# Performance work log

Hardware: AMD Instinct MI355X
Metric: run time of the kernel (lower is better)

The kernel has to match this reference:

```python
import jax, jax.numpy as jnp
import numpy as np

D = 768; HID = 3072; FFN = 2048; NH = 8; NL = 2; T = 64; V = 50257; B = 16
ALPHA = 0.4; HD = D // NH

def _gelu(x):
    return jax.nn.gelu(x, approximate=False)

def _ln(x, g, b, eps=1e-5):
    m = x.mean(-1, keepdims=True)
    v = x.var(-1, keepdims=True)
    return (x - m) / jnp.sqrt(v + eps) * g + b

def _l2norm(x):
    return x / jnp.maximum(jnp.linalg.norm(x, axis=-1, keepdims=True), 1e-12)

def _mha(x, in_w, in_b, out_w, out_b, mask):
    b, t, _ = x.shape
    qkv = x @ in_w.T + in_b
    q, k, v = jnp.split(qkv, 3, axis=-1)
    q = q.reshape(b, t, NH, HD); k = k.reshape(b, t, NH, HD); v = v.reshape(b, t, NH, HD)
    s = jnp.einsum('bqhd,bkhd->bhqk', q, k) / jnp.sqrt(jnp.asarray(HD, jnp.float32))
    s = jnp.where(mask[None, None], -jnp.inf, s)
    a = jax.nn.softmax(s, axis=-1)
    o = jnp.einsum('bhqk,bkhd->bqhd', a, v).reshape(b, t, D)
    return o @ out_w.T + out_b

def _forward(token_ids, emb, pos_emb, attn_in_w, attn_in_b, attn_out_w, attn_out_b,
             ff_w1, ff_b1, ff_w2, ff_b2, n1_g, n1_b, n2_g, n2_b, enc_norm_g, enc_norm_b,
             V0, b0, V1, b1, cp_w1, cp_b1, cp_w2, cp_b2, gate_w, gate_b, temp_w, R,
             out_g, out_b, lm_head):
    sg = jax.lax.stop_gradient
    x = emb[token_ids] + pos_emb[None, :token_ids.shape[1]]
    t = token_ids.shape[1]
    mask = jnp.triu(jnp.ones((t, t), bool), 1)
    for l in range(NL):
        xn = _ln(x, n1_g[l], n1_b[l])
        x = x + _mha(xn, attn_in_w[l], attn_in_b[l], attn_out_w[l], attn_out_b[l], mask)
        xn = _ln(x, n2_g[l], n2_b[l])
        x = x + _gelu(xn @ ff_w1[l].T + ff_b1[l]) @ ff_w2[l].T + ff_b2[l]
    ctx = _l2norm(_ln(x, enc_norm_g, enc_norm_b))  # [B,T,D]

    def step(h_prev, ctx_t):
        h_d = sg(h_prev)                      # h_prev.detach()
        traw = h_d @ R                        # temporal_raw
        tc = ctx_t + ALPHA * traw             # temporal_context
        # differentiable shadow path through hierarchy weights V0,b0,V1,b1
        h_sh = _gelu(tc @ V0 + b0)
        core_sh = _l2norm(_gelu(h_sh @ V1 + b1))
        # settled state: hierarchy inference under no_grad (settle approximated
        # by the same feedforward pass; fully stop-gradiented like x.detach())
        tcd = sg(tc)
        core_set = sg(_l2norm(_gelu(_gelu(tcd @ V0 + b0) @ V1 + b1)))
        blend = 0.5 * core_sh + 0.5 * core_set
        cf = _gelu(blend @ cp_w1.T + cp_b1) @ cp_w2.T + cp_b2   # core_proj
        tf = traw @ temp_w.T                                     # temporal_proj
        gate = jax.nn.sigmoid(jnp.concatenate([ctx_t, cf], -1) @ gate_w.T + gate_b)
        h_t = gate * (cf + ALPHA * tf) + (1.0 - gate) * ctx_t    # gate_warmup=1.0
        h_t = jnp.clip(_ln(h_t, out_g, out_b), -5.0, 5.0)
        return sg(h_t), h_t @ lm_head.T

    h0 = jnp.zeros((token_ids.shape[0], D), jnp.float32)
    _, logits = jax.lax.scan(step, h0, jnp.swapaxes(ctx, 0, 1))
    return jnp.transpose(logits, (1, 0, 2))

def setup_inputs():
    key = jax.random.key(0)
    ks = iter(jax.random.split(key, 64))
    def nrm(shape, s=0.02):
        return jax.random.normal(next(ks), shape, jnp.float32) * s
    return {
        'token_ids': jax.random.randint(next(ks), (B, T), 0, V),
        'emb': nrm((V, D)),
        'pos_emb': nrm((T, D)),
        'attn_in_w': nrm((NL, 3 * D, D)),
        'attn_in_b': jnp.zeros((NL, 3 * D), jnp.float32),
        'attn_out_w': nrm((NL, D, D)),
        'attn_out_b': jnp.zeros((NL, D), jnp.float32),
        'ff_w1': nrm((NL, FFN, D)),
        'ff_b1': jnp.zeros((NL, FFN), jnp.float32),
        'ff_w2': nrm((NL, D, FFN)),
        'ff_b2': jnp.zeros((NL, D), jnp.float32),
        'n1_g': jnp.ones((NL, D), jnp.float32),
        'n1_b': jnp.zeros((NL, D), jnp.float32),
        'n2_g': jnp.ones((NL, D), jnp.float32),
        'n2_b': jnp.zeros((NL, D), jnp.float32),
        'enc_norm_g': jnp.ones((D,), jnp.float32),
        'enc_norm_b': jnp.zeros((D,), jnp.float32),
        'V0': nrm((D, HID)),
        'b0': jnp.zeros((HID,), jnp.float32),
        'V1': nrm((HID, D)),
        'b1': jnp.zeros((D,), jnp.float32),
        'cp_w1': nrm((D, D)),
        'cp_b1': jnp.zeros((D,), jnp.float32),
        'cp_w2': nrm((D, D)),
        'cp_b2': jnp.zeros((D,), jnp.float32),
        'gate_w': nrm((D, 2 * D)),
        'gate_b': jnp.zeros((D,), jnp.float32),
        'temp_w': nrm((D, D)),
        'R': nrm((D, D), 0.1),
        'out_g': jnp.ones((D,), jnp.float32),
        'out_b': jnp.zeros((D,), jnp.float32),
        'lm_head': nrm((V, D)),
    }

def reference(token_ids, emb, pos_emb, attn_in_w, attn_in_b, attn_out_w, attn_out_b,
              ff_w1, ff_b1, ff_w2, ff_b2, n1_g, n1_b, n2_g, n2_b, enc_norm_g, enc_norm_b,
              V0, b0, V1, b1, cp_w1, cp_b1, cp_w2, cp_b2, gate_w, gate_b, temp_w, R,
              out_g, out_b, lm_head):
    return _forward(token_ids, emb, pos_emb, attn_in_w, attn_in_b, attn_out_w, attn_out_b,
                    ff_w1, ff_b1, ff_w2, ff_b2, n1_g, n1_b, n2_g, n2_b, enc_norm_g, enc_norm_b,
                    V0, b0, V1, b1, cp_w1, cp_b1, cp_w2, cp_b2, gate_w, gate_b, temp_w, R,
                    out_g, out_b, lm_head)
```

## Files before the change

### kernel.cpp

```cpp
#include <hip/hip_runtime.h>
#include <math.h>

typedef _Float16 f16;
typedef f16 f16x8 __attribute__((ext_vector_type(8)));
typedef f16 f16x4 __attribute__((ext_vector_type(4)));
typedef float f32x4 __attribute__((ext_vector_type(4)));
typedef unsigned int u32;
typedef unsigned long long u64;

#define TT 64
#define DD 768
#define MR 1024
#define ALPHAF 0.4f
#define NWG 120
#define GRID 240
#define LMN 50257
#define LMK 768

__device__ __forceinline__ float geluf(float x){
  return 0.5f*x*(1.0f + erff(x*0.70710678118654752f));
}

__device__ __forceinline__ u64 ld_a64(const void* p){
  return __hip_atomic_load((const u64*)p, __ATOMIC_RELAXED, __HIP_MEMORY_SCOPE_AGENT);
}
__device__ __forceinline__ f16x8 ld_act16h(const f16* p){
  union { u64 u[2]; f16x8 v; } c;
  c.u[0] = ld_a64(p); c.u[1] = ld_a64(p + 4); return c.v;
}
__device__ __forceinline__ float ld_actf(const float* p){
  union { u32 u; float f; } c;
  c.u = __hip_atomic_load((const u32*)p, __ATOMIC_RELAXED, __HIP_MEMORY_SCOPE_AGENT);
  return c.f;
}
__device__ __forceinline__ void st_actf(float* p, float v){
  union { u32 u; float f; } c; c.f = v;
  __hip_atomic_store((u32*)p, c.u, __ATOMIC_RELAXED, __HIP_MEMORY_SCOPE_AGENT);
}
__device__ __forceinline__ void st_acth(f16* p, float v){
  union { unsigned short u; f16 h; } c; c.h = (f16)v;
  __hip_atomic_store((unsigned short*)p, c.u, __ATOMIC_RELAXED, __HIP_MEMORY_SCOPE_AGENT);
}

__device__ __forceinline__ void egbar(int* ef, int ep){
  __syncthreads();
  if (threadIdx.x == 0){
    __threadfence();
    __hip_atomic_store(ef + blockIdx.x*32, ep, __ATOMIC_RELAXED, __HIP_MEMORY_SCOPE_AGENT);
  }
  {
    int id = threadIdx.x; bool active = id < GRID;
    const int* fp = ef + id*32;
    while (true){
      int v = active ? __hip_atomic_load(fp, __ATOMIC_RELAXED, __HIP_MEMORY_SCOPE_AGENT) : ep;
      if (__ballot(v >= ep) == ~0ull) break;
      __builtin_amdgcn_s_sleep(1);
    }
  }
  __syncthreads();
  if (threadIdx.x == 0) __threadfence();
  __syncthreads();
}

__device__ __forceinline__ void postf(int* f, int ep){
  asm volatile("s_waitcnt vmcnt(0)" ::: "memory");
  __syncthreads();
  if (threadIdx.x == 0)
    __hip_atomic_store(f, ep, __ATOMIC_RELAXED, __HIP_MEMORY_SCOPE_AGENT);
}
__device__ __forceinline__ void waitf(const int* f, int n, int ep){
  if (threadIdx.x < 64){
    int lane = threadIdx.x;
    while (true){
      bool ok = true;
      for (int i = lane; i < n; i += 64){
        if (__hip_atomic_load(f + i*32, __ATOMIC_RELAXED, __HIP_MEMORY_SCOPE_AGENT) < ep){
          ok = false; break;
        }
      }
      if (__ballot(ok) == ~0ull) break;
      __builtin_amdgcn_s_sleep(1);
    }
  }
  __syncthreads();
}

__device__ __forceinline__ void red_store(float* rb, int lane, f32x4 a){
  rb[lane] = a[0]; rb[64+lane] = a[1]; rb[128+lane] = a[2]; rb[192+lane] = a[3];
}
__device__ __forceinline__ f32x4 red_sum4(float rb[4][256], int lane){
  f32x4 s;
  #pragma unroll
  for (int r = 0; r < 4; r++)
    s[r] = rb[0][r*64+lane] + rb[1][r*64+lane] + rb[2][r*64+lane] + rb[3][r*64+lane];
  return s;
}
__device__ __forceinline__ f32x4 red_sum2(float rb[4][256], int lane, int w0, int w1){
  f32x4 s;
  #pragma unroll
  for (int r = 0; r < 4; r++)
    s[r] = rb[w0][r*64+lane] + rb[w1][r*64+lane];
  return s;
}

__device__ void dev_ln(const float* xr, const float* g, const float* b,
                       float* outr, float* outTr, float* red, bool l2n){
  int tid = threadIdx.x, lane = tid & 63, wid = tid >> 6;
  float v[3]; float s = 0.f, ss = 0.f;
  #pragma unroll
  for (int j = 0; j < 3; j++){ float t0 = xr[tid + j*256]; v[j] = t0; s += t0; ss += t0*t0; }
  #pragma unroll
  for (int o = 1; o < 64; o <<= 1){ s += __shfl_xor(s, o); ss += __shfl_xor(ss, o); }
  if (lane == 0){ red[wid] = s; red[4+wid] = ss; }
  __syncthreads();
  s  = red[0]+red[1]+red[2]+red[3];
  ss = red[4]+red[5]+red[6]+red[7];
  float mean = s*(1.f/768.f);
  float var  = ss*(1.f/768.f) - mean*mean;
  float rstd = rsqrtf(var + 1e-5f);
  float y[3];
  #pragma unroll
  for (int j = 0; j < 3; j++){ int n = tid + j*256; y[j] = (v[j]-mean)*rstd*g[n] + b[n]; }
  if (l2n){
    float n2 = y[0]*y[0] + y[1]*y[1] + y[2]*y[2];
    #pragma unroll
    for (int o = 1; o < 64; o <<= 1) n2 += __shfl_xor(n2, o);
    __syncthreads();
    if (lane == 0) red[wid] = n2;
    __syncthreads();
    n2 = red[0]+red[1]+red[2]+red[3];
    float inv = 1.f / fmaxf(sqrtf(n2), 1e-12f);
    y[0] *= inv; y[1] *= inv; y[2] *= inv;
  }
  #pragma unroll
  for (int j = 0; j < 3; j++) outr[tid + j*256] = y[j];
  if (outTr){
    #pragma unroll
    for (int j = 0; j < 3; j++) outTr[tid + j*256] = y[j];
  }
  __syncthreads();
}

__device__ void dev_gemm_tile(char* lds, const float* A, int lda,
    const float* Bw, int ldb, int nrb, int N, int K, int m0, int n0,
    const float* bias, const float* res, float* outF, f16* outH,
    float scale, int act, int operm)
{
  int tid = threadIdx.x;
  int lane = tid & 63, wid = tid >> 6;
  int wr = (wid >> 1)*64, wc = (wid & 1)*64;
  int l15 = lane & 15, kb = lane >> 4;
  f32x4 acc[4][4];
  #pragma unroll
  for (int i = 0; i < 4; i++)
    #pragma unroll
    for (int j = 0; j < 4; j++){ f32x4 z = {0.f,0.f,0.f,0.f}; acc[i][j] = z; }
  int rA = tid >> 3;
  int k4 = (tid & 7)*4;
  float4 va[4], vb[4];
  #pragma unroll
  for (int it = 0; it < 4; ++it){
    int r = it*32 + rA;
    va[it] = *(const float4*)(A + (size_t)(m0+r)*lda + k4);
    int rB = n0 + r;
    if (rB < nrb) vb[it] = *(const float4*)(Bw + (size_t)rB*ldb + k4);
    else { vb[it].x=0.f; vb[it].y=0.f; vb[it].z=0.f; vb[it].w=0.f; }
  }
  for (int kk = 0; kk < K; kk += 32){
    char* cb = lds + (((kk >> 5) & 1) ? 20480 : 0);
    f16 (*As)[40] = (f16(*)[40])cb;
    f16 (*Bs)[40] = (f16(*)[40])(cb + 10240);
    #pragma unroll
    for (int it = 0; it < 4; ++it){
      int r = it*32 + rA;
      *(f16x4*)(&As[r][k4]) = (f16x4){(f16)va[it].x,(f16)va[it].y,(f16)va[it].z,(f16)va[it].w};
      *(f16x4*)(&Bs[r][k4]) = (f16x4){(f16)vb[it].x,(f16)vb[it].y,(f16)vb[it].z,(f16)vb[it].w};
    }
    __syncthreads();
    if (kk + 32 < K){
      #pragma unroll
      for (int it = 0; it < 4; ++it){
        int r = it*32 + rA;
        va[it] = *(const float4*)(A + (size_t)(m0+r)*lda + kk + 32 + k4);
        int rB = n0 + r;
        if (rB < nrb) vb[it] = *(const float4*)(Bw + (size_t)rB*ldb + kk + 32 + k4);
        else { vb[it].x=0.f; vb[it].y=0.f; vb[it].z=0.f; vb[it].w=0.f; }
      }
    }
    f16x8 af[4], bfv[4];
    #pragma unroll
    for (int i = 0; i < 4; i++) af[i]  = *(const f16x8*)(&As[wr + i*16 + l15][kb*8]);
    #pragma unroll
    for (int j = 0; j < 4; j++) bfv[j] = *(const f16x8*)(&Bs[wc + j*16 + l15][kb*8]);
    #pragma unroll
    for (int i = 0; i < 4; i++)
      #pragma unroll
      for (int j = 0; j < 4; j++)
        acc[i][j] = __builtin_amdgcn_mfma_f32_16x16x32_f16(af[i], bfv[j], acc[i][j], 0, 0, 0);
  }
  __syncthreads();
  #pragma unroll
  for (int i = 0; i < 4; i++){
    #pragma unroll
    for (int j = 0; j < 4; j++){
      #pragma unroll
      for (int r = 0; r < 4; r++){
        int m = m0 + wr + i*16 + kb*4 + r;
        int n = n0 + wc + j*16 + l15;
        if (n < N){
          float v = acc[i][j][r]*scale;
          if (bias) v += bias[n];
          if (act == 1) v = geluf(v);
          if (res) v += res[(size_t)m*N + n];
          size_t off;
          if (operm == 0) off = (size_t)m*N + n;
          else            off = ((size_t)(m & 63)*16 + (m >> 6))*N + n;
          if (outF) outF[off] = v;
          if (outH) outH[off] = (f16)v;
        }
      }
    }
  }
}

__device__ void dev_attn(char* lds, const float* qkv, float* o, int bh){
  float (*kv)[96] = (float(*)[96])lds;
  float (*sm)[68] = (float(*)[68])(lds + 24576);
  int b = bh >> 3, h = bh & 7;
  int tid = threadIdx.x;
  const float* base = qkv + (size_t)b*64*2304 + h*96;
  for (int idx = tid; idx < 64*96; idx += 256){ int i = idx/96, d = idx - i*96;
    kv[i][d] = base[(size_t)i*2304 + 768 + d]; }
  __syncthreads();
  {
    int i = tid >> 2;
    const float* q = base + (size_t)i*2304;
    int j0 = (tid & 3)*16;
    for (int jj = 0; jj < 16; jj++){
      int j = j0 + jj;
      float sv = -1e30f;
      if (j <= i){ float acc = 0.f;
        for (int d = 0; d < 96; d++) acc += q[d]*kv[j][d];
        sv = acc*0.10206207261596576f; }
      sm[i][j] = sv;
    }
  }
  __syncthreads();
  for (int idx = tid; idx < 64*96; idx += 256){ int i = idx/96, d = idx - i*96;
    kv[i][d] = base[(size_t)i*2304 + 1536 + d]; }
  if (tid < 64){
    int i = tid;
    float mx = -1e30f;
    for (int j = 0; j <= i; j++) mx = fmaxf(mx, sm[i][j]);
    float sum = 0.f;
    for (int j = 0; j <= i; j++){ float e = expf(sm[i][j]-mx); sm[i][j] = e; sum += e; }
    float inv = 1.f/sum;
    for (int j = 0; j <= i; j++) sm[i][j] *= inv;
  }
  __syncthreads();
  for (int idx = tid; idx < 64*96; idx += 256){
    int i = idx/96, d = idx - i*96;
    float acc = 0.f;
    for (int j = 0; j <= i; j++) acc += sm[i][j]*kv[j][d];
    o[(size_t)(b*64+i)*768 + h*96 + d] = acc;
  }
  __syncthreads();
}

__device__ void dev_tr_f(char* lds, const float* in, float* out, int R, int C, int bx, int by){
  float (*tile)[33] = (float(*)[33])lds;
  int r0 = by*32, c0 = bx*32;
  int tx = threadIdx.x & 31, ty = threadIdx.x >> 5;
  #pragma unroll
  for (int i = 0; i < 32; i += 8) tile[ty+i][tx] = in[(size_t)(r0+ty+i)*C + (c0+tx)];
  __syncthreads();
  #pragma unroll
  for (int i = 0; i < 32; i += 8) out[(size_t)(c0+ty+i)*R + (r0+tx)] = tile[tx][ty+i];
  __syncthreads();
}
__device__ void dev_tr_h(char* lds, const float* in, f16* out, int R, int C, int bx, int by){
  float (*tile)[33] = (float(*)[33])lds;
  int r0 = by*32, c0 = bx*32;
  int tx = threadIdx.x & 31, ty = threadIdx.x >> 5;
  #pragma unroll
  for (int i = 0; i < 32; i += 8) tile[ty+i][tx] = in[(size_t)(r0+ty+i)*C + (c0+tx)];
  __syncthreads();
  #pragma unroll
  for (int i = 0; i < 32; i += 8) out[(size_t)(c0+ty+i)*R + (r0+tx)] = (f16)tile[tx][ty+i];
  __syncthreads();
}

__global__ void k_init(int* flags){
  for (int i = threadIdx.x; i < 512*32; i += 256) flags[i] = 0;
}

__global__ __launch_bounds__(256, 1) void k_all(
  const int* tok, const float* emb, const float* pos,
  const float* aiw, const float* aib, const float* aow, const float* aob,
  const float* fw1, const float* fb1, const float* fw2, const float* fb2,
  const float* n1g, const float* n1b, const float* n2g, const float* n2b,
  const float* eng, const float* enb,
  const float* V0, const float* b0, const float* V1, const float* b1,
  const float* cw1, const float* cb1, const float* cw2, const float* cb2,
  const float* gw, const float* gb_, const float* tw, const float* Rm,
  const float* og, const float* ob, const float* lmw,
  float* x, float* xn, float* qkv, float* o_, float* mid,
  float* ctx, float* ctxT, float* V0t, float* cw2t,
  float* ctxV0T, float* gctxT, float* bdg,
  f16* WAf, f16* V1tf, f16* Wc1f, f16* WDf, f16* lmw16,
  f16* hf, f16* h1f, f16* c1f, f16* gcaf,
  float* cf, float* gpre, float* tfs, int* flags, float* out)
{
  __shared__ __align__(16) char smem[147456];
  __shared__ float redbuf[4][256];
  __shared__ float normp[4][16];
  __shared__ float red[8];
  const int tid = threadIdx.x, lane = tid & 63, wid = tid >> 6;
  const int bid = blockIdx.x;
  const int l15 = lane & 15, kb = lane >> 4;
  int* afl = flags;
  int* bfl = flags + 120*32;
  int* cfl = flags + 168*32;
  int* dfl = flags + 192*32;
  int* mfl = flags + 240*32;
  int* encf = flags + 256*32;
  int eep = 0;

  for (int m = bid; m < MR; m += GRID){
    int t = m & 63; int id = tok[m];
    const float* e = emb + (size_t)id*DD;
    const float* p = pos + (size_t)t*DD;
    float* xr = x + (size_t)m*DD;
    for (int j = tid; j < DD; j += 256) xr[j] = e[j] + p[j];
  }
  egbar(encf, ++eep);

  for (int l = 0; l < 2; l++){
    for (int m = bid; m < MR; m += GRID)
      dev_ln(x + (size_t)m*DD, n1g + l*DD, n1b + l*DD, xn + (size_t)m*DD, nullptr, red, false);
    egbar(encf, ++eep);
    for (int tl = bid; tl < 144; tl += GRID)
      dev_gemm_tile(smem, xn, 768, aiw + (size_t)l*2304*768, 768, 2304, 2304, 768,
                    (tl % 8)*128, (tl / 8)*128, aib + l*2304, nullptr, qkv, nullptr, 1.f, 0, 0);
    egbar(encf, ++eep);
    for (int u = bid; u < 128; u += GRID) dev_attn(smem, qkv, o_, u);
    egbar(encf, ++eep);
    for (int tl = bid; tl < 48; tl += GRID)
      dev_gemm_tile(smem, o_, 768, aow + (size_t)l*768*768, 768, 768, 768, 768,
                    (tl % 8)*128, (tl / 8)*128, aob + l*768, x, x, nullptr, 1.f, 0, 0);
    egbar(encf, ++eep);
    for (int m = bid; m < MR; m += GRID)
      dev_ln(x + (size_t)m*DD, n2g + l*DD, n2b + l*DD, xn + (size_t)m*DD, nullptr, red, false);
    egbar(encf, ++eep);
    for (int tl = bid; tl < 128; tl += GRID)
      dev_gemm_tile(smem, xn, 768, fw1 + (size_t)l*2048*768, 768, 2048, 2048, 768,
                    (tl % 8)*128, (tl / 8)*128, fb1 + l*2048, nullptr, mid, nullptr, 1.f, 1, 0);
    egbar(encf, ++eep);
    for (int tl = bid; tl < 48; tl += GRID)
      dev_gemm_tile(smem, mid, 2048, fw2 + (size_t)l*768*2048, 2048, 768, 768, 2048,
                    (tl % 8)*128, (tl / 8)*128, fb2 + l*768, x, x, nullptr, 1.f, 0, 0);
    egbar(encf, ++eep);
  }
  for (int m = bid; m < MR; m += GRID)
    dev_ln(x + (size_t)m*DD, eng, enb, ctx + (size_t)m*DD,
           ctxT + ((size_t)(m & 63)*16 + (m >> 6))*DD, red, true);
  egbar(encf, ++eep);

  for (int task = bid; task < 5184; task += GRID){
    if (task < 2304)      dev_tr_f(smem, V0, V0t, 768, 3072, task % 96, task / 96);
    else if (task < 2880){ int t2 = task - 2304; dev_tr_f(smem, cw2, cw2t, 768, 768, t2 % 24, t2 / 24); }
    else                 { int t2 = task - 2880; dev_tr_h(smem, V1, V1tf, 3072, 768, t2 % 24, t2 / 24); }
  }
  {
    const int g0 = bid*256 + tid, stride = GRID*256;
    for (int i = g0; i < 73728; i += stride){
      float4 a = ((const float4*)cw1)[i*2]; float4 b2 = ((const float4*)cw1)[i*2+1];
      ((f16x8*)Wc1f)[i] = (f16x8){(f16)a.x,(f16)a.y,(f16)a.z,(f16)a.w,(f16)b2.x,(f16)b2.y,(f16)b2.z,(f16)b2.w};
    }
    for (int i = g0; i < 73728; i += stride){
      float4 a = ((const float4*)cw2)[i*2]; float4 b2 = ((const float4*)cw2)[i*2+1];
      ((f16x8*)WDf)[i] = (f16x8){(f16)a.x,(f16)a.y,(f16)a.z,(f16)a.w,(f16)b2.x,(f16)b2.y,(f16)b2.z,(f16)b2.w};
    }
    for (int g = g0; g < 768; g += stride){
      const float* row = gw + (size_t)g*1536 + 768;
      float s = 0.f;
      for (int j = 0; j < 768; j++) s += cb2[j]*row[j];
      bdg[g] = s;
    }
  }
  egbar(encf, ++eep);

  for (int task = bid; task < 456; task += GRID){
    if (task < 144)
      dev_gemm_tile(smem, V0t, 768, Rm, 768, 768, 768, 768,
                    (task % 24)*128, (task / 24)*128, nullptr, nullptr, nullptr, WAf, ALPHAF, 0, 0);
    else if (task < 180){ int t2 = task - 144;
      dev_gemm_tile(smem, tw, 768, Rm, 768, 768, 768, 768,
                    (t2 % 6)*128, (t2 / 6)*128, nullptr, nullptr, nullptr, WAf + (size_t)3072*768, ALPHAF, 0, 0); }
    else if (task < 372){ int t2 = task - 180;
      dev_gemm_tile(smem, ctx, 768, V0t, 768, 3072, 3072, 768,
                    (t2 % 8)*128, (t2 / 8)*128, b0, nullptr, ctxV0T, nullptr, 1.f, 0, 1); }
    else if (task < 420){ int t2 = task - 372;
      dev_gemm_tile(smem, ctx, 768, gw, 1536, 768, 768, 768,
                    (t2 % 8)*128, (t2 / 8)*128, nullptr, nullptr, gctxT, nullptr, 1.f, 0, 1); }
    else { int t2 = task - 420;
      dev_gemm_tile(smem, gw + 768, 1536, cw2t, 768, 768, 768, 768,
                    (t2 % 6)*128, (t2 / 6)*128, nullptr, nullptr, nullptr, WDf + (size_t)768*768, 1.f, 0, 0); }
  }
  egbar(encf, ++eep);

  if (bid >= NWG){
    const int lw = bid - NWG;
    const int wr = (wid >> 1)*64, wc = (wid & 1)*64;
    for (int nt = lw; nt < 393; nt += 120){
      int r0 = nt*128;
      int rend = r0 + 128; if (rend > LMN) rend = LMN;
      int u0 = r0*96, u1 = rend*96;
      for (int i = u0 + tid; i < u1; i += 256){
        float4 a = ((const float4*)lmw)[(size_t)i*2];
        float4 b2 = ((const float4*)lmw)[(size_t)i*2+1];
        ((f16x8*)lmw16)[i] = (f16x8){(f16)a.x,(f16)a.y,(f16)a.z,(f16)a.w,
                                     (f16)b2.x,(f16)b2.y,(f16)b2.z,(f16)b2.w};
      }
    }
    __syncthreads();
    for (int q = 0; q < 8; ++q){
      waitf(mfl, 16, q*8 + 8);
      size_t arow[4];
      #pragma unroll
      for (int i = 0; i < 4; i++){
        int rl = wr + i*16 + l15;
        arow[i] = ((size_t)(rl >> 3)*TT + q*8 + (rl & 7))*DD + kb*8;
      }
      for (int nt = lw; nt < 393; nt += 120){
        int n0 = nt*128;
        size_t brow[4];
        #pragma unroll
        for (int j = 0; j < 4; j++){
          int n = n0 + wc + j*16 + l15;
          if (n > LMN-1) n = LMN-1;
          brow[j] = (size_t)n*LMK + kb*8;
        }
        f32x4 acc[4][4];
        #pragma unroll
        for (int i = 0; i < 4; i++)
          #pragma unroll
          for (int j = 0; j < 4; j++){ f32x4 z = {0.f,0.f,0.f,0.f}; acc[i][j] = z; }
        #pragma unroll 4
        for (int kk = 0; kk < LMK; kk += 32){
          f16x8 af[4], bf[4];
          #pragma unroll
          for (int i = 0; i < 4; i++) af[i] = ld_act16h(hf + arow[i] + kk);
          #pragma unroll
          for (int j = 0; j < 4; j++) bf[j] = *(const f16x8*)(lmw16 + brow[j] + kk);
          #pragma unroll
          for (int i = 0; i < 4; i++)
            #pragma unroll
            for (int j = 0; j < 4; j++)
              acc[i][j] = __builtin_amdgcn_mfma_f32_16x16x32_f16(af[i], bf[j], acc[i][j], 0, 0, 0);
        }
        #pragma unroll
        for (int i = 0; i < 4; i++){
          #pragma unroll
          for (int j = 0; j < 4; j++){
            #pragma unroll
            for (int r = 0; r < 4; r++){
              int ml = wr + i*16 + kb*4 + r;
              int b = ml >> 3, tt = q*8 + (ml & 7);
              int n = n0 + wc + j*16 + l15;
              if (n < LMN) out[((size_t)b*TT + tt)*LMN + n] = acc[i][j][r];
            }
          }
        }
      }
    }
    return;
  }

  {
    const f16* src = WAf + (size_t)bid*32*768;
    for (int c = tid; c < 3072; c += 256){
      int row = c/96, kc = c - row*96;
      int off = (row*1536 + kc*16) ^ ((row&7)<<4);
      *(f16x8*)(smem + off) = *(const f16x8*)(src + (size_t)row*768 + kc*8);
    }
    if (bid < 48){
      const f16* s2 = V1tf + (size_t)bid*16*3072;
      for (int c = tid; c < 6144; c += 256){
        int row = c/384, kc = c - row*384;
        int off = (row*6144 + kc*16) ^ ((row&7)<<4);
        *(f16x8*)(smem + 49152 + off) = *(const f16x8*)(s2 + (size_t)row*3072 + kc*8);
      }
    } else if (bid < 72){
      const f16* s2 = Wc1f + (size_t)(bid-48)*32*768;
      for (int c = tid; c < 3072; c += 256){
        int row = c/96, kc = c - row*96;
        int off = (row*1536 + kc*16) ^ ((row&7)<<4);
        *(f16x8*)(smem + 49152 + off) = *(const f16x8*)(s2 + (size_t)row*768 + kc*8);
      }
    } else {
      const f16* s2 = WDf + (size_t)(bid-72)*32*768;
      for (int c = tid; c < 3072; c += 256){
        int row = c/96, kc = c - row*96;
        int off = (row*1536 + kc*16) ^ ((row&7)<<4);
        *(f16x8*)(smem + 49152 + off) = *(const f16x8*)(s2 + (size_t)row*768 + kc*8);
      }
    }
  }
  __syncthreads();

  const int n_a = bid*32 + (wid>>1)*16 + l15;
  float b1v = 0.f;
  if (bid < 48) b1v = b1[bid*16 + l15];
  float cpb1v = 0.f;
  if (bid >= 48 && bid < 72) cpb1v = cb1[((bid-48)*2 + (wid>>1))*16 + l15];
  float dbv = 0.f; int n_d = 0;
  if (bid >= 72){
    n_d = ((bid-72)*2 + (wid>>1))*16 + l15;
    dbv = (n_d < 768) ? cb2[n_d] : bdg[n_d - 768];
  }
  float gb3[3], og3[3], ob3[3];
  if (bid < 16){
    #pragma unroll
    for (int j = 0; j < 3; j++){
      int n = tid + j*256;
      gb3[j] = gb_[n]; og3[j] = og[n]; ob3[j] = ob[n];
    }
  }

  for (int t = 0; t < TT; ++t){
    const int ep = t + 1;
    f32x4 cv = {0.f,0.f,0.f,0.f};
    if ((wid & 1) == 0 && n_a < 3072){
      const float* p = ctxV0T + (size_t)t*16*3072 + n_a;
      #pragma unroll
      for (int r = 0; r < 4; r++) cv[r] = p[(size_t)(kb*4+r)*3072];
    }

    if (t > 0) waitf(mfl, 16, t);
    {
      const int u = wid >> 1, kh = wid & 1;
      const int k0 = kh*384 + kb*8;
      f32x4 a = {0.f,0.f,0.f,0.f};
      if (t > 0){
        const f16* ap = hf + ((size_t)l15*TT + (t-1))*DD + k0;
        const int row = u*16 + l15, rowoff = row*1536, sw = (row&7)<<4;
        #pragma unroll
        for (int b = 0; b < 12; b++){
          int wb = (rowoff + (k0 + b*32)*2) ^ sw;
          f16x8 vb = *(const f16x8*)(smem + wb);
          f16x8 va = ld_act16h(ap + b*32);
          a = __builtin_amdgcn_mfma_f32_16x16x32_f16(va, vb, a, 0,0,0);
        }
      }
      red_store(redbuf[wid], lane, a);
    }
    __syncthreads();
    if ((wid & 1) == 0){
      f32x4 s4 = red_sum2(redbuf, lane, wid, wid+1);
      #pragma unroll
      for (int r = 0; r < 4; r++){
        int m = kb*4 + r;
        if (n_a < 3072){
          float hv = geluf(s4[r] + cv[r]);
          st_acth(h1f + (size_t)m*3072 + n_a, hv);
        } else {
          st_actf(tfs + m*DD + (n_a - 3072), s4[r]);
        }
      }
    }
    postf(afl + bid*32, ep);
    if (bid < 48){
      waitf(afl, 120, ep);
      const int k0 = wid*768 + kb*8;
      const f16* ap = h1f + (size_t)l15*3072 + k0;
      const int rowoff = l15*6144, sw = (l15&7)<<4;
      f32x4 a = {0.f,0.f,0.f,0.f};
      #pragma unroll
      for (int b = 0; b < 24; b++){
        int wb = (rowoff + (k0 + b*32)*2) ^ sw;
        f16x8 vb = *(const f16x8*)(smem + 49152 + wb);
        f16x8 va = ld_act16h(ap + b*32);
        a = __builtin_amdgcn_mfma_f32_16x16x32_f16(va, vb, a, 0,0,0);
      }
      red_store(redbuf[wid], lane, a);
      __syncthreads();
      if (wid == 0){
        f32x4 s4 = red_sum4(redbuf, lane);
        int n = bid*16 + l15;
        #pragma unroll
        for (int r = 0; r < 4; r++){
          int m = kb*4 + r;
          st_acth(c1f + (size_t)m*DD + n, geluf(s4[r] + b1v));
        }
      }
      postf(bfl + bid*32, ep);
    }
    float gv[3], cxv[3];
    if (bid < 16){
      #pragma unroll
      for (int j = 0; j < 3; j++){
        size_t o2 = ((size_t)t*16 + bid)*DD + tid + j*256;
        gv[j] = gctxT[o2]; cxv[j] = ctxT[o2];
      }
    }
    if (bid >= 48 && bid < 72){
      waitf(bfl, 48, ep);
      const int u = wid >> 1, kh = wid & 1;
      const int k0 = kh*384 + kb*8;
      const f16* ap = c1f + (size_t)l15*DD + k0;
      const int row = u*16 + l15, rowoff = row*1536, sw = (row&7)<<4;
      f32x4 a = {0.f,0.f,0.f,0.f};
      float sq = 0.f;
      #pragma unroll
      for (int b = 0; b < 12; b++){
        int wb = (rowoff + (k0 + b*32)*2) ^ sw;
        f16x8 vb = *(const f16x8*)(smem + 49152 + wb);
        f16x8 va = ld_act16h(ap + b*32);
        a = __builtin_amdgcn_mfma_f32_16x16x32_f16(va, vb, a, 0,0,0);
        #pragma unroll
        for (int j = 0; j < 8; j++){ float xv = (float)va[j]; sq = fmaf(xv, xv, sq); }
      }
      sq += __shfl_xor(sq,16); sq += __shfl_xor(sq,32);
      if (lane < 16) normp[wid][lane] = sq;
      red_store(redbuf[wid], lane, a);
      __syncthreads();
      if ((wid & 1) == 0){
        f32x4 s4 = red_sum2(redbuf, lane, wid, wid+1);
        int n = ((bid-48)*2 + (wid>>1))*16 + l15;
        #pragma unroll
        for (int r = 0; r < 4; r++){
          int m = kb*4 + r;
          float nm = normp[wid][m] + normp[wid+1][m];
          float inv = 1.f / fmaxf(sqrtf(nm), 1e-12f);
          st_acth(gcaf + (size_t)m*DD + n, geluf(s4[r]*inv + cpb1v));
        }
      }
      postf(cfl + (bid-48)*32, ep);
    }
    if (bid >= 72){
      waitf(cfl, 24, ep);
      const int u = wid >> 1, kh = wid & 1;
      const int k0 = kh*384 + kb*8;
      const f16* ap = gcaf + (size_t)l15*DD + k0;
      const int row = u*16 + l15, rowoff = row*1536, sw = (row&7)<<4;
      f32x4 a = {0.f,0.f,0.f,0.f};
      #pragma unroll
      for (int b = 0; b < 12; b++){
        int wb = (rowoff + (k0 + b*32)*2) ^ sw;
        f16x8 vb = *(const f16x8*)(smem + 49152 + wb);
        f16x8 va = ld_act16h(ap + b*32);
        a = __builtin_amdgcn_mfma_f32_16x16x32_f16(va, vb, a, 0,0,0);
      }
      red_store(redbuf[wid], lane, a);
      __syncthreads();
      if ((wid & 1) == 0){
        f32x4 s4 = red_sum2(redbuf, lane, wid, wid+1);
        #pragma unroll
        for (int r = 0; r < 4; r++){
          int m = kb*4 + r;
          if (n_d < 768) st_actf(cf + m*DD + n_d, s4[r] + dbv);
          else           st_actf(gpre + m*DD + (n_d - 768), s4[r] + dbv);
        }
      }
      postf(dfl + (bid-72)*32, ep);
    }
    if (bid < 16){
      waitf(dfl, 48, ep);
      int m = bid;
      float vals[3]; float s = 0.f, ss = 0.f;
      #pragma unroll
      for (int j = 0; j < 3; j++){
        int n = tid + j*256;
        float gi = gv[j] + ld_actf(gpre + m*DD + n) + gb3[j];
        float gate = 1.f/(1.f + expf(-gi));
        float v = gate*(ld_actf(cf + m*DD + n) + ld_actf(tfs + m*DD + n)) + (1.f - gate)*cxv[j];
        vals[j] = v; s += v; ss += v*v;
      }
      #pragma unroll
      for (int o2 = 1; o2 < 64; o2 <<= 1){ s += __shfl_xor(s, o2); ss += __shfl_xor(ss, o2); }
      if (lane == 0){ red[wid] = s; red[4+wid] = ss; }
      __syncthreads();
      s  = red[0]+red[1]+red[2]+red[3];
      ss = red[4]+red[5]+red[6]+red[7];
      float mean = s*(1.f/768.f), var = ss*(1.f/768.f) - mean*mean;
      float rstd = rsqrtf(var + 1e-5f);
      #pragma unroll
      for (int j = 0; j < 3; j++){
        int n = tid + j*256;
        float y = (vals[j]-mean)*rstd*og3[j] + ob3[j];
        y = fminf(5.f, fmaxf(-5.f, y));
        st_acth(hf + ((size_t)m*TT + t)*DD + n, y);
      }
      postf(mfl + bid*32, ep);
    }
  }
}

extern "C" void kernel_launch(void* const* d_in, const int* in_sizes, int n_in,
                              void* d_out, int out_size, void* d_ws, size_t ws_size,
                              hipStream_t stream)
{
  (void)in_sizes; (void)n_in; (void)out_size; (void)ws_size;
  const int*   tok = (const int*)d_in[0];
  const float* emb = (const float*)d_in[1];
  const float* pos = (const float*)d_in[2];
  const float* aiw = (const float*)d_in[3];
  const float* aib = (const float*)d_in[4];
  const float* aow = (const float*)d_in[5];
  const float* aob = (const float*)d_in[6];
  const float* fw1 = (const float*)d_in[7];
  const float* fb1 = (const float*)d_in[8];
  const float* fw2 = (const float*)d_in[9];
  const float* fb2 = (const float*)d_in[10];
  const float* n1g = (const float*)d_in[11];
  const float* n1b = (const float*)d_in[12];
  const float* n2g = (const float*)d_in[13];
  const float* n2b = (const float*)d_in[14];
  const float* eng = (const float*)d_in[15];
  const float* enb = (const float*)d_in[16];
  const float* V0  = (const float*)d_in[17];
  const float* b0  = (const float*)d_in[18];
  const float* V1  = (const float*)d_in[19];
  const float* b1  = (const float*)d_in[20];
  const float* cw1 = (const float*)d_in[21];
  const float* cb1 = (const float*)d_in[22];
  const float* cw2 = (const float*)d_in[23];
  const float* cb2 = (const float*)d_in[24];
  const float* gw  = (const float*)d_in[25];
  const float* gb  = (const float*)d_in[26];
  const float* tw  = (const float*)d_in[27];
  const float* Rm  = (const float*)d_in[28];
  const float* og  = (const float*)d_in[29];
  const float* ob  = (const float*)d_in[30];
  const float* lmw = (const float*)d_in[31];
  float* out = (float*)d_out;

  char* base = (char*)d_ws; size_t off = 0;
  auto alloc = [&](size_t bytes)->void*{
    off = (off + 255) & ~(size_t)255; void* p = base + off; off += bytes; return p; };

  float* x     = (float*)alloc((size_t)MR*DD*4);
  float* xn    = (float*)alloc((size_t)MR*DD*4);
  float* qkv   = (float*)alloc((size_t)MR*2304*4);
  float* o_    = (float*)alloc((size_t)MR*DD*4);
  float* mid   = (float*)alloc((size_t)MR*2048*4);
  float* ctx   = (float*)alloc((size_t)MR*DD*4);
  float* ctxT  = (float*)alloc((size_t)MR*DD*4);
  float* V0t   = (float*)alloc((size_t)3072*768*4);
  float* cw2t  = (float*)alloc((size_t)768*768*4);
  float* ctxV0T= (float*)alloc((size_t)MR*3072*4);
  float* gctxT = (float*)alloc((size_t)MR*DD*4);
  float* bdg   = (float*)alloc(768*4);
  f16*   WAf   = (f16*)alloc((size_t)3840*768*2);
  f16*   V1tf  = (f16*)alloc((size_t)768*3072*2);
  f16*   Wc1f  = (f16*)alloc((size_t)768*768*2);
  f16*   WDf   = (f16*)alloc((size_t)1536*768*2);
  f16*   lmw16 = (f16*)alloc((size_t)LMN*768*2);
  f16*   hf    = (f16*)alloc((size_t)MR*DD*2);
  f16*   h1f   = (f16*)alloc((size_t)16*3072*2);
  f16*   c1f   = (f16*)alloc((size_t)16*768*2);
  f16*   gcaf  = (f16*)alloc((size_t)16*768*2);
  float* cf    = (float*)alloc((size_t)16*768*4);
  float* gpre  = (float*)alloc((size_t)16*768*4);
  float* tfs   = (float*)alloc((size_t)16*768*4);
  int*   flags = (int*)alloc((size_t)512*32*4);

  k_init<<<1, 256, 0, stream>>>(flags);
  k_all<<<GRID, 256, 0, stream>>>(tok, emb, pos, aiw, aib, aow, aob,
      fw1, fb1, fw2, fb2, n1g, n1b, n2g, n2b, eng, enb,
      V0, b0, V1, b1, cw1, cb1, cw2, cb2, gw, gb, tw, Rm, og, ob, lmw,
      x, xn, qkv, o_, mid, ctx, ctxT, V0t, cw2t, ctxV0T, gctxT, bdg,
      WAf, V1tf, Wc1f, WDf, lmw16, hf, h1f, c1f, gcaf, cf, gpre, tfs, flags, out);
}
```

Before: 2.698 ms.

## Fuse gating and LayerNorm partial stats into D-stage, remove serial epilogue barrier

The gate, blend and partial LayerNorm sums are now computed inside the D-stage workgroups. Each writes its values and per-slice sum/sumsq into a 4-slot ring buffer. The next timestep's A-stage reconstructs mean/rstd from those partials and applies the LayerNorm on the fly while loading its MFMA operand. This removes one cross-workgroup barrier hop per recurrent step, the separate 16-block LN stage. The LM-head workgroups now materialise hf for the lm_head GEMM off the critical path. The cost is extra redundant LN arithmetic in the A-stage, a ring-buffer dependency (D waits on mfl t-3), and a less stable variance formula.

```diff
diff --git a/kernel.cpp b/kernel.cpp
--- a/kernel.cpp
+++ b/kernel.cpp
@@ -27,6 +27,9 @@
 __device__ __forceinline__ f16x8 ld_act16h(const f16* p){
   union { u64 u[2]; f16x8 v; } c;
   c.u[0] = ld_a64(p); c.u[1] = ld_a64(p + 4); return c.v;
+}
+__device__ __forceinline__ float2 ld_actf2(const float* p){
+  union { u64 u; float2 f; } c; c.u = ld_a64(p); return c.f;
 }
 __device__ __forceinline__ float ld_actf(const float* p){
   union { u32 u; float f; } c;
@@ -309,7 +312,7 @@
   float* ctxV0T, float* gctxT, float* bdg,
   f16* WAf, f16* V1tf, f16* Wc1f, f16* WDf, f16* lmw16,
   f16* hf, f16* h1f, f16* c1f, f16* gcaf,
-  float* cf, float* gpre, float* tfs, int* flags, float* out)
+  float* val, float* pp, float* tfs, int* flags, float* out)
 {
   __shared__ __align__(16) char smem[147456];
   __shared__ float redbuf[4][256];
@@ -424,53 +427,131 @@
       }
     }
     __syncthreads();
-    for (int q = 0; q < 8; ++q){
-      waitf(mfl, 16, q*8 + 8);
-      size_t arow[4];
-      #pragma unroll
-      for (int i = 0; i < 4; i++){
-        int rl = wr + i*16 + l15;
-        arow[i] = ((size_t)(rl >> 3)*TT + q*8 + (rl & 7))*DD + kb*8;
-      }
-      for (int nt = lw; nt < 393; nt += 120){
-        int n0 = nt*128;
-        size_t brow[4];
+
+    if (lw < 16){
+      const int m = lw;
+      for (int t = 0; t < TT; ++t){
+        waitf(dfl, 48, t+1);
+        const int slot = t & 3;
+        if (tid < 64){
+          float s = 0.f, ss = 0.f;
+          if (lane < 48){
+            float2 v2 = ld_actf2(pp + slot*1536 + m*96 + lane*2);
+            s = v2.x; ss = v2.y;
+          }
+          #pragma unroll
+          for (int o2 = 1; o2 < 64; o2 <<= 1){ s += __shfl_xor(s, o2); ss += __shfl_xor(ss, o2); }
+          if (lane == 0){ red[0] = s; red[1] = ss; }
+        }
+        __syncthreads();
+        float mean = red[0]*(1.f/768.f);
+        float rstd = rsqrtf(red[1]*(1.f/768.f) - mean*mean + 1e-5f);
         #pragma unroll
-        for (int j = 0; j < 4; j++){
-          int n = n0 + wc + j*16 + l15;
-          if (n > LMN-1) n = LMN-1;
-          brow[j] = (size_t)n*LMK + kb*8;
-        }
-        f32x4 acc[4][4];
+        for (int j = 0; j < 3; j++){
+          int n = tid + j*256;
+          float v = ld_actf(val + slot*12288 + m*768 + n);
+          float y = (v - mean)*rstd*og[n] + ob[n];
+          y = fminf(5.f, fmaxf(-5.f, y));
+          st_acth(hf + ((size_t)m*TT + t)*DD + n, y);
+        }
+        postf(mfl + m*32, t+1);
+        if ((t & 7) == 7){
+          int q = t >> 3;
+          waitf(mfl, 16, t+1);
+          size_t arow[4];
+          #pragma unroll
+          for (int i = 0; i < 4; i++){
+            int rl = wr + i*16 + l15;
+            arow[i] = ((size_t)(rl >> 3)*TT + q*8 + (rl & 7))*DD + kb*8;
+          }
+          for (int nt = lw; nt < 393; nt += 120){
+            int n0 = nt*128;
+            size_t brow[4];
+            #pragma unroll
+            for (int j = 0; j < 4; j++){
+              int n = n0 + wc + j*16 + l15;
+              if (n > LMN-1) n = LMN-1;
+              brow[j] = (size_t)n*LMK + kb*8;
+            }
+            f32x4 acc[4][4];
+            #pragma unroll
+            for (int i = 0; i < 4; i++)
+              #pragma unroll
+              for (int j = 0; j < 4; j++){ f32x4 z = {0.f,0.f,0.f,0.f}; acc[i][j] = z; }
+            #pragma unroll 4
+            for (int kk = 0; kk < LMK; kk += 32){
+              f16x8 af[4], bf[4];
+              #pragma unroll
+              for (int i = 0; i < 4; i++) af[i] = ld_act16h(hf + arow[i] + kk);
+              #pragma unroll
+              for (int j = 0; j < 4; j++) bf[j] = *(const f16x8*)(lmw16 + brow[j] + kk);
+              #pragma unroll
+              for (int i = 0; i < 4; i++)
+                #pragma unroll
+                for (int j = 0; j < 4; j++)
+                  acc[i][j] = __builtin_amdgcn_mfma_f32_16x16x32_f16(af[i], bf[j], acc[i][j], 0, 0, 0);
+            }
+            #pragma unroll
+            for (int i = 0; i < 4; i++)
+              #pragma unroll
+              for (int j = 0; j < 4; j++)
+                #pragma unroll
+                for (int r = 0; r < 4; r++){
+                  int ml = wr + i*16 + kb*4 + r;
+                  int b = ml >> 3, tt2 = q*8 + (ml & 7);
+                  int n = n0 + wc + j*16 + l15;
+                  if (n < LMN) out[((size_t)b*TT + tt2)*LMN + n] = acc[i][j][r];
+                }
+          }
+        }
+      }
+    } else {
+      for (int q = 0; q < 8; ++q){
+        waitf(mfl, 16, q*8 + 8);
+        size_t arow[4];
         #pragma unroll
-        for (int i = 0; i < 4; i++)
+        for (int i = 0; i < 4; i++){
+          int rl = wr + i*16 + l15;
+          arow[i] = ((size_t)(rl >> 3)*TT + q*8 + (rl & 7))*DD + kb*8;
+        }
+        for (int nt = lw; nt < 393; nt += 120){
+          int n0 = nt*128;
+          size_t brow[4];
           #pragma unroll
-          for (int j = 0; j < 4; j++){ f32x4 z = {0.f,0.f,0.f,0.f}; acc[i][j] = z; }
-        #pragma unroll 4
-        for (int kk = 0; kk < LMK; kk += 32){
-          f16x8 af[4], bf[4];
+          for (int j = 0; j < 4; j++){
+            int n = n0 + wc + j*16 + l15;
+            if (n > LMN-1) n = LMN-1;
+            brow[j] = (size_t)n*LMK + kb*8;
+          }
+          f32x4 acc[4][4];
           #pragma unroll
-          for (int i = 0; i < 4; i++) af[i] = ld_act16h(hf + arow[i] + kk);
-          #pragma unroll
-          for (int j = 0; j < 4; j++) bf[j] = *(const f16x8*)(lmw16 + brow[j] + kk);
+          for (int i = 0; i < 4; i++)
+            #pragma unroll
+            for (int j = 0; j < 4; j++){ f32x4 z = {0.f,0.f,0.f,0.f}; acc[i][j] = z; }
+          #pragma unroll 4
+          for (int kk = 0; kk < LMK; kk += 32){
+            f16x8 af[4], bf[4];
+            #pragma unroll
+            for (int i = 0; i < 4; i++) af[i] = ld_act16h(hf + arow[i] + kk);
+            #pragma unroll
+            for (int j = 0; j < 4; j++) bf[j] = *(const f16x8*)(lmw16 + brow[j] + kk);
+            #pragma unroll
+            for (int i = 0; i < 4; i++)
+              #pragma unroll
+              for (int j = 0; j < 4; j++)
+                acc[i][j] = __builtin_amdgcn_mfma_f32_16x16x32_f16(af[i], bf[j], acc[i][j], 0, 0, 0);
+          }
           #pragma unroll
           for (int i = 0; i < 4; i++)
             #pragma unroll
             for (int j = 0; j < 4; j++)
-              acc[i][j] = __builtin_amdgcn_mfma_f32_16x16x32_f16(af[i], bf[j], acc[i][j], 0, 0, 0);
-        }
-        #pragma unroll
-        for (int i = 0; i < 4; i++){
-          #pragma unroll
-          for (int j = 0; j < 4; j++){
-            #pragma unroll
-            for (int r = 0; r < 4; r++){
-              int ml = wr + i*16 + kb*4 + r;
-              int b = ml >> 3, tt = q*8 + (ml & 7);
-              int n = n0 + wc + j*16 + l15;
-              if (n < LMN) out[((size_t)b*TT + tt)*LMN + n] = acc[i][j][r];
-            }
-          }
+              #pragma unroll
+              for (int r = 0; r < 4; r++){
+                int ml = wr + i*16 + kb*4 + r;
+                int b = ml >> 3, tt2 = q*8 + (ml & 7);
+                int n = n0 + wc + j*16 + l15;
+                if (n < LMN) out[((size_t)b*TT + tt2)*LMN + n] = acc[i][j][r];
+              }
         }
       }
     }
@@ -499,11 +580,12 @@
         *(f16x8*)(smem + 49152 + off) = *(const f16x8*)(s2 + (size_t)row*768 + kc*8);
       }
     } else {
-      const f16* s2 = WDf + (size_t)(bid-72)*32*768;
+      int u = bid - 72;
       for (int c = tid; c < 3072; c += 256){
         int row = c/96, kc = c - row*96;
+        int grow = (row < 16) ? (u*16 + row) : (768 + u*16 + (row - 16));
         int off = (row*1536 + kc*16) ^ ((row&7)<<4);
-        *(f16x8*)(smem + 49152 + off) = *(const f16x8*)(s2 + (size_t)row*768 + kc*8);
+        *(f16x8*)(smem + 49152 + off) = *(const f16x8*)(WDf + (size_t)grow*768 + kc*8);
       }
     }
   }
@@ -514,18 +596,10 @@
   if (bid < 48) b1v = b1[bid*16 + l15];
   float cpb1v = 0.f;
   if (bid >= 48 && bid < 72) cpb1v = cb1[((bid-48)*2 + (wid>>1))*16 + l15];
-  float dbv = 0.f; int n_d = 0;
+  float cbv = 0.f, bdgv = 0.f, gbv = 0.f; int n_d2 = 0;
   if (bid >= 72){
-    n_d = ((bid-72)*2 + (wid>>1))*16 + l15;
-    dbv = (n_d < 768) ? cb2[n_d] : bdg[n_d - 768];
-  }
-  float gb3[3], og3[3], ob3[3];
-  if (bid < 16){
-    #pragma unroll
-    for (int j = 0; j < 3; j++){
-      int n = tid + j*256;
-      gb3[j] = gb_[n]; og3[j] = og[n]; ob3[j] = ob[n];
-    }
+    n_d2 = (bid-72)*16 + l15;
+    cbv = cb2[n_d2]; bdgv = bdg[n_d2]; gbv = gb_[n_d2];
   }
 
   for (int t = 0; t < TT; ++t){
@@ -537,19 +611,45 @@
       for (int r = 0; r < 4; r++) cv[r] = p[(size_t)(kb*4+r)*3072];
     }
 
-    if (t > 0) waitf(mfl, 16, t);
+    if (t > 0) waitf(dfl, 48, t);
     {
       const int u = wid >> 1, kh = wid & 1;
       const int k0 = kh*384 + kb*8;
       f32x4 a = {0.f,0.f,0.f,0.f};
       if (t > 0){
-        const f16* ap = hf + ((size_t)l15*TT + (t-1))*DD + k0;
+        const int slot = (t-1) & 3;
+        float s = 0.f, ss = 0.f;
+        {
+          int m = lane & 15, q = lane >> 4;
+          const float* pq = pp + slot*1536 + m*96 + q*24;
+          #pragma unroll
+          for (int j = 0; j < 12; j++){ float2 v2 = ld_actf2(pq + j*2); s += v2.x; ss += v2.y; }
+        }
+        s += __shfl_xor(s,16); ss += __shfl_xor(ss,16);
+        s += __shfl_xor(s,32); ss += __shfl_xor(ss,32);
+        float mean = s*(1.f/768.f);
+        float rstd = rsqrtf(ss*(1.f/768.f) - mean*mean + 1e-5f);
+        const float* vp = val + slot*12288 + (size_t)l15*768;
         const int row = u*16 + l15, rowoff = row*1536, sw = (row&7)<<4;
         #pragma unroll
         for (int b = 0; b < 12; b++){
-          int wb = (rowoff + (k0 + b*32)*2) ^ sw;
+          int kc = k0 + b*32;
+          float2 e0 = ld_actf2(vp+kc), e1 = ld_actf2(vp+kc+2);
+          float2 e2 = ld_actf2(vp+kc+4), e3 = ld_actf2(vp+kc+6);
+          float4 g0 = *(const float4*)(og+kc), g1 = *(const float4*)(og+kc+4);
+          float4 o0 = *(const float4*)(ob+kc), o1 = *(const float4*)(ob+kc+4);
+          float vv[8] = {e0.x,e0.y,e1.x,e1.y,e2.x,e2.y,e3.x,e3.y};
+          float gg[8] = {g0.x,g0.y,g0.z,g0.w,g1.x,g1.y,g1.z,g1.w};
+          float oo[8] = {o0.x,o0.y,o0.z,o0.w,o1.x,o1.y,o1.z,o1.w};
+          f16x8 va;
+          #pragma unroll
+          for (int j = 0; j < 8; j++){
+            float y = (vv[j]-mean)*rstd*gg[j] + oo[j];
+            y = fminf(5.f, fmaxf(-5.f, y));
+            va[j] = (f16)y;
+          }
+          int wb = (rowoff + kc*2) ^ sw;
           f16x8 vb = *(const f16x8*)(smem + wb);
-          f16x8 va = ld_act16h(ap + b*32);
           a = __builtin_amdgcn_mfma_f32_16x16x32_f16(va, vb, a, 0,0,0);
         }
       }
@@ -595,14 +695,6 @@
         }
       }
       postf(bfl + bid*32, ep);
-    }
-    float gv[3], cxv[3];
-    if (bid < 16){
-      #pragma unroll
-      for (int j = 0; j < 3; j++){
-        size_t o2 = ((size_t)t*16 + bid)*DD + tid + j*256;
-        gv[j] = gctxT[o2]; cxv[j] = ctxT[o2];
-      }
     }
     if (bid >= 48 && bid < 72){
       waitf(bfl, 48, ep);
@@ -640,10 +732,11 @@
     }
     if (bid >= 72){
       waitf(cfl, 24, ep);
-      const int u = wid >> 1, kh = wid & 1;
+      if (t >= 4) waitf(mfl, 16, t - 3);
+      const int isg = wid >> 1, kh = wid & 1;
       const int k0 = kh*384 + kb*8;
       const f16* ap = gcaf + (size_t)l15*DD + k0;
-      const int row = u*16 + l15, rowoff = row*1536, sw = (row&7)<<4;
+      const int row = isg*16 + l15, rowoff = row*1536, sw = (row&7)<<4;
       f32x4 a = {0.f,0.f,0.f,0.f};
       #pragma unroll
       for (int b = 0; b < 12; b++){
@@ -654,45 +747,38 @@
       }
       red_store(redbuf[wid], lane, a);
       __syncthreads();
-      if ((wid & 1) == 0){
-        f32x4 s4 = red_sum2(redbuf, lane, wid, wid+1);
+      if (wid == 0){
+        const int u = bid - 72, slot = t & 3;
+        f32x4 acf = red_sum2(redbuf, lane, 0, 1);
+        f32x4 agp = red_sum2(redbuf, lane, 2, 3);
+        int n = u*16 + l15;
+        float valr[4];
         #pragma unroll
         for (int r = 0; r < 4; r++){
           int m = kb*4 + r;
-          if (n_d < 768) st_actf(cf + m*DD + n_d, s4[r] + dbv);
-          else           st_actf(gpre + m*DD + (n_d - 768), s4[r] + dbv);
+          size_t gi_idx = ((size_t)t*16 + m)*DD + n;
+          float cfv = acf[r] + cbv;
+          float gpv = agp[r] + bdgv;
+          float gi  = gctxT[gi_idx] + gpv + gbv;
+          float gate = 1.f/(1.f + expf(-gi));
+          float tf = ld_actf(tfs + m*DD + n);
+          float vv = gate*(cfv + tf) + (1.f - gate)*ctxT[gi_idx];
+          st_actf(val + slot*12288 + m*768 + n, vv);
+          valr[r] = vv;
+        }
+        #pragma unroll
+        for (int r = 0; r < 4; r++){
+          float s2 = valr[r], ss2 = valr[r]*valr[r];
+          #pragma unroll
+          for (int o2 = 1; o2 < 16; o2 <<= 1){ s2 += __shfl_xor(s2, o2); ss2 += __shfl_xor(ss2, o2); }
+          if (l15 == 0){
+            int m = kb*4 + r;
+            st_actf(pp + slot*1536 + m*96 + u*2,     s2);
+            st_actf(pp + slot*1536 + m*96 + u*2 + 1, ss2);
+          }
         }
       }
       postf(dfl + (bid-72)*32, ep);
-    }
-    if (bid < 16){
-      waitf(dfl, 48, ep);
-      int m = bid;
-      float vals[3]; float s = 0.f, ss = 0.f;
-      #pragma unroll
-      for (int j = 0; j < 3; j++){
-        int n = tid + j*256;
-        float gi = gv[j] + ld_actf(gpre + m*DD + n) + gb3[j];
-        float gate = 1.f/(1.f + expf(-gi));
-        float v = gate*(ld_actf(cf + m*DD + n) + ld_actf(tfs + m*DD + n)) + (1.f - gate)*cxv[j];
-        vals[j] = v; s += v; ss += v*v;
-      }
-      #pragma unroll
-      for (int o2 = 1; o2 < 64; o2 <<= 1){ s += __shfl_xor(s, o2); ss += __shfl_xor(ss, o2); }
-      if (lane == 0){ red[wid] = s; red[4+wid] = ss; }
-      __syncthreads();
-      s  = red[0]+red[1]+red[2]+red[3];
-      ss = red[4]+red[5]+red[6]+red[7];
-      float mean = s*(1.f/768.f), var = ss*(1.f/768.f) - mean*mean;
-      float rstd = rsqrtf(var + 1e-5f);
-      #pragma unroll
-      for (int j = 0; j < 3; j++){
-        int n = tid + j*256;
-        float y = (vals[j]-mean)*rstd*og3[j] + ob3[j];
-        y = fminf(5.f, fmaxf(-5.f, y));
-        st_acth(hf + ((size_t)m*TT + t)*DD + n, y);
-      }
-      postf(mfl + bid*32, ep);
     }
   }
 }
@@ -761,8 +847,8 @@
   f16*   h1f   = (f16*)alloc((size_t)16*3072*2);
   f16*   c1f   = (f16*)alloc((size_t)16*768*2);
   f16*   gcaf  = (f16*)alloc((size_t)16*768*2);
-  float* cf    = (float*)alloc((size_t)16*768*4);
-  float* gpre  = (float*)alloc((size_t)16*768*4);
+  float* val   = (float*)alloc((size_t)4*16*768*4);
+  float* pp    = (float*)alloc((size_t)4*16*96*4);
   float* tfs   = (float*)alloc((size_t)16*768*4);
   int*   flags = (int*)alloc((size_t)512*32*4);
 
@@ -771,5 +857,5 @@
       fw1, fb1, fw2, fb2, n1g, n1b, n2g, n2b, eng, enb,
       V0, b0, V1, b1, cw1, cb1, cw2, cb2, gw, gb, tw, Rm, og, ob, lmw,
       x, xn, qkv, o_, mid, ctx, ctxT, V0t, cw2t, ctxV0T, gctxT, bdg,
-      WAf, V1tf, Wc1f, WDf, lmw16, hf, h1f, c1f, gcaf, cf, gpre, tfs, flags, out);
-}
+      WAf, V1tf, Wc1f, WDf, lmw16, hf, h1f, c1f, gcaf, val, pp, tfs, flags, out);
+}
```

Measured after the change: 3.118 ms. 15.6% more time.
